# Kernel tuning notes

Hardware: AMD Instinct MI355X
Metric: run time of the kernel (lower is better)

## Reference

```python
import jax, jax.numpy as jnp
import numpy as np

N_POST_NMS = 2000      # Config.train_n_nms
MIN_SIZE = 16.0        # Config.prop_min_size
IMG_H = 800.0          # Config.input_shape[0]
IMG_W = 800.0          # Config.input_shape[1]
NMS_THRESH = 0.7       # Config.nms_thresh
N_PROPOSALS = 8192


def setup_inputs() -> dict:
    key = jax.random.key(0)
    k1, k2, k3 = jax.random.split(key, 3)
    # bbox_locs rows are (cy, cx, h, w); make them plausible for an 800x800 image
    ctr = jax.random.uniform(k1, (N_PROPOSALS, 2), dtype=jnp.float32) * 800.0
    sz = jax.random.uniform(k2, (N_PROPOSALS, 2), dtype=jnp.float32) * 260.0 + 4.0
    bbox_locs = jnp.concatenate([ctr, sz], axis=1)
    object_scores = jax.random.uniform(k3, (N_PROPOSALS,), dtype=jnp.float32)
    return {"bbox_locs": bbox_locs, "object_scores": object_scores}


def _decode_clip(bbox_locs):
    # center/size -> corners (y1,x1,y2,x2), size filter BEFORE clipping (as in source)
    cy, cx, h, w = bbox_locs[:, 0], bbox_locs[:, 1], bbox_locs[:, 2], bbox_locs[:, 3]
    y1, x1 = cy - 0.5 * h, cx - 0.5 * w
    y2, x2 = cy + 0.5 * h, cx + 0.5 * w
    valid = ((y2 - y1) > MIN_SIZE) & ((x2 - x1) > MIN_SIZE)
    boxes = jnp.stack([
        jnp.clip(y1, 0.0, IMG_H),
        jnp.clip(x1, 0.0, IMG_W),
        jnp.clip(y2, 0.0, IMG_H),
        jnp.clip(x2, 0.0, IMG_W),
    ], axis=1)  # [N,4]
    return boxes, valid


def _iou_matrix(b):
    # pairwise IoU, same convention as tf.image.non_max_suppression (no +1)
    y1, x1, y2, x2 = b[:, 0], b[:, 1], b[:, 2], b[:, 3]
    area = (y2 - y1) * (x2 - x1)
    iy = jnp.maximum(0.0, jnp.minimum(y2[:, None], y2[None, :]) - jnp.maximum(y1[:, None], y1[None, :]))
    ix = jnp.maximum(0.0, jnp.minimum(x2[:, None], x2[None, :]) - jnp.maximum(x1[:, None], x1[None, :]))
    inter = iy * ix
    union = area[:, None] + area[None, :] - inter
    return jnp.where(union > 0.0, inter / union, 0.0)


def _nms_select(boxes, scores, valid):
    # Greedy NMS. Invalid (too-small) boxes get -inf score so they sort last and
    # start suppressed -- equivalent to the tf.gather filtering in the original.
    N = boxes.shape[0]
    order = jnp.argsort(-jnp.where(valid, scores, -jnp.inf))
    bs = boxes[order]
    iou = _iou_matrix(bs)  # [N,N]
    idx = jnp.arange(N)

    def body(i, state):
        suppressed, kept = state
        keep_i = jnp.logical_not(suppressed[i])
        kept = kept.at[i].set(keep_i)
        suppressed = suppressed | (keep_i & (iou[i] > NMS_THRESH) & (idx > i))
        return suppressed, kept

    suppressed0 = jnp.logical_not(valid[order])
    kept0 = jnp.zeros((N,), dtype=bool)
    _, kept = jax.lax.fori_loop(0, N, body, (suppressed0, kept0))

    # first N_POST_NMS kept boxes in score order (same as max_output_size in TF)
    sel = jnp.nonzero(kept, size=N_POST_NMS, fill_value=0)[0]
    out_valid = jnp.arange(N_POST_NMS) < jnp.sum(kept)
    return order[sel], out_valid


def reference(bbox_locs, object_scores):
    boxes, valid = _decode_clip(bbox_locs)
    sel_idx, out_valid = _nms_select(boxes, object_scores, valid)
    # pad slots beyond the number of kept boxes with zeros (fixed output shape)
    return jnp.where(out_valid[:, None], boxes[sel_idx], 0.0)
```

## Files before the change

kernel.cpp:

```cpp
#include <hip/hip_runtime.h>
#include <cstdint>
#include <cstddef>

typedef unsigned long long ull;
typedef unsigned short u16;

#define N 8192
#define NWORDS 128
#define NPOST 2000
#define NMS_THR 0.7f
#define MASKW 48
#define SCAP 128
#define ICAP 16
#define NUNITS 312
#define SLICE_STRIDE 260


__device__ __forceinline__ float4 decode_clip_box(const float4 L, bool* valid) {
#pragma clang fp contract(off)
  float cy = L.x, cx = L.y, h = L.z, w = L.w;
  float y1 = cy - 0.5f * h;
  float x1 = cx - 0.5f * w;
  float y2 = cy + 0.5f * h;
  float x2 = cx + 0.5f * w;
  *valid = ((y2 - y1) > 16.0f) && ((x2 - x1) > 16.0f);
  float4 b;
  b.x = fminf(fmaxf(y1, 0.0f), 800.0f);
  b.y = fminf(fmaxf(x1, 0.0f), 800.0f);
  b.z = fminf(fmaxf(y2, 0.0f), 800.0f);
  b.w = fminf(fmaxf(x2, 0.0f), 800.0f);
  return b;
}

__device__ __forceinline__ float box_area(const float4 b) {
#pragma clang fp contract(off)
  return (b.z - b.x) * (b.w - b.y);
}

__device__ __forceinline__ bool iou_gt_thr(const float4 a, float aa,
                                           const float4 b, float ab) {
#pragma clang fp contract(off)
  float iy = fminf(a.z, b.z) - fmaxf(a.x, b.x);
  float ix = fminf(a.w, b.w) - fmaxf(a.y, b.y);
  iy = fmaxf(iy, 0.0f);
  ix = fmaxf(ix, 0.0f);
  float inter = iy * ix;
  float uni = aa + ab - inter;
  return (inter > 0.0f) && (uni > 0.0f) && ((inter / uni) > NMS_THR);
}

__device__ __forceinline__ ull resolve_word(ull dg, ull avail, int lane) {
  ull conflict = __ballot(((dg & avail) != 0ull) && ((avail >> lane) & 1ull));
  if (conflict == 0ull) return avail;
  ull dgT = 0ull;
  #pragma unroll
  for (int c = 0; c < 64; ++c) {
    ull tb = __ballot((dg >> c) & 1ull);
    if (lane == c) dgT = tb;
  }
  ull kept = avail;
  while (true) {
    bool sup = (dgT & kept) != 0ull;
    ull kn = avail & ~__ballot(sup);
    if (kn == kept) break;
    kept = kn;
  }
  return kept;
}

__device__ __forceinline__ unsigned aload(const unsigned* p) {
  return __hip_atomic_load(p, __ATOMIC_RELAXED, __HIP_MEMORY_SCOPE_AGENT);
}
__device__ __forceinline__ int aloadi(const int* p) {
  return __hip_atomic_load(p, __ATOMIC_RELAXED, __HIP_MEMORY_SCOPE_AGENT);
}

__global__ __launch_bounds__(256) void rankgather_kernel(
    const float* __restrict__ locs, const float* __restrict__ scores,
    float4* __restrict__ bs, float* __restrict__ area,
    int* __restrict__ ctrl, int* __restrict__ inCnt) {
  __shared__ float ssc[32 * SLICE_STRIDE];
  __shared__ int sRank[8][33];
  int tid = threadIdx.x, bid = blockIdx.x;
  if (bid == 0) {
    if (tid < 64) ctrl[tid] = 0;
    else if (tid < 128) inCnt[tid - 64] = 0;
  }
  const float4* locs4 = (const float4*)locs;
  for (int k = 0; k < 32; ++k) {
    int j = k * 256 + tid;
    bool v; (void)decode_clip_box(locs4[j], &v);
    float s = v ? scores[j] : -__builtin_inff();
    ssc[(j >> 8) * SLICE_STRIDE + (j & 255)] = s;
  }
  __syncthreads();
  int boxOff = tid & 7;
  int part = tid >> 3;
  int i = bid * 8 + boxOff;
  float si = ssc[(i >> 8) * SLICE_STRIDE + (i & 255)];
  const float4* s4 = (const float4*)(ssc + part * SLICE_STRIDE);
  int j0 = part * 256;
  int cnt = 0;
  for (int q = 0; q < 64; ++q) {
    float4 v = s4[q];
    int j = j0 + 4 * q;
    cnt += (v.x > si) || ((v.x == si) & ((j + 0) < i));
    cnt += (v.y > si) || ((v.y == si) & ((j + 1) < i));
    cnt += (v.z > si) || ((v.z == si) & ((j + 2) < i));
    cnt += (v.w > si) || ((v.w == si) & ((j + 3) < i));
  }
  sRank[boxOff][part] = cnt;
  __syncthreads();
  if (tid < 8) {
    int r = 0;
    #pragma unroll
    for (int p = 0; p < 32; ++p) r += sRank[tid][p];
    int ig = bid * 8 + tid;
    bool v;
    float4 b = decode_clip_box(locs4[ig], &v);
    bs[r] = b;
    area[r] = v ? box_area(b) : -1.0f;
  }
}

__global__ __launch_bounds__(256) void pairscan_kernel(
    const float4* __restrict__ bs, const float* __restrict__ area,
    int* __restrict__ ctrl, int* __restrict__ inCnt,
    unsigned* __restrict__ srcBuf, unsigned* __restrict__ inBuf,
    float* __restrict__ out) {
  __shared__ __align__(16) char smem[35840];
  int tid = threadIdx.x, bid = blockIdx.x;

  if (bid > 0) {
    float4* sb = (float4*)smem;
    float*  sa = (float*)(smem + 4096);
    int u = bid - 1;
    int cbq = 0;
    while (2 * (cbq + 1) * (cbq + 2) <= u) ++cbq;
    int rb = u - 2 * cbq * (cbq + 1);
    int lane = tid & 63, cq = tid >> 6;
    int cb = cbq * 4 + cq;
    int j0 = cb * 64;
    sb[cq * 64 + lane] = bs[j0 + lane];
    sa[cq * 64 + lane] = area[j0 + lane];
    int i = rb * 64 + lane;
    float4 r = bs[i];
    float ai = area[i];
    __syncthreads();
    if (cb >= rb && ai >= 0.0f) {
      ull bits = 0;
      for (int c = 0; c < 64; ++c) {
        if ((j0 + c) > i && sa[cq * 64 + c] >= 0.0f &&
            iou_gt_thr(r, ai, sb[cq * 64 + c], sa[cq * 64 + c]))
          bits |= 1ull << c;
      }
      int n = (int)__popcll(bits);
      if (n) {
        if (cb == rb) {
          int base = atomicAdd(&inCnt[cb], n);
          if (base + n > ICAP) {
            __hip_atomic_store(&ctrl[48], 1, __ATOMIC_RELAXED,
                               __HIP_MEMORY_SCOPE_AGENT);
          } else {
            int k = base;
            while (bits) {
              int c = (int)__builtin_ctzll(bits); bits &= bits - 1;
              __hip_atomic_store(&inBuf[cb * ICAP + k++],
                                 ((unsigned)c << 8) | (unsigned)lane,
                                 __ATOMIC_RELAXED, __HIP_MEMORY_SCOPE_AGENT);
            }
          }
        } else {
          int base = atomicAdd(&ctrl[rb], n);
          if (base + n > SCAP) {
            __hip_atomic_store(&ctrl[48], 1, __ATOMIC_RELAXED,
                               __HIP_MEMORY_SCOPE_AGENT);
          } else {
            int k = base;
            while (bits) {
              int c = (int)__builtin_ctzll(bits); bits &= bits - 1;
              __hip_atomic_store(&srcBuf[rb * SCAP + k++],
                                 ((unsigned)lane << 13) | ((unsigned)cb << 6) |
                                     (unsigned)c,
                                 __ATOMIC_RELAXED, __HIP_MEMORY_SCOPE_AGENT);
            }
          }
        }
      }
    }
    __syncthreads();
    if (tid == 0)
      __hip_atomic_fetch_add(&ctrl[49], 1, __ATOMIC_RELAXED,
                             __HIP_MEMORY_SCOPE_AGENT);
    return;
  }

  unsigned (*sSrc)[SCAP] = (unsigned(*)[SCAP])(smem + 0);
  unsigned (*sIn)[ICAP]  = (unsigned(*)[ICAP])(smem + 24576);
  int*  sSCnt     = (int*)(smem + 27648);
  int*  sICnt     = (int*)(smem + 27840);
  ull*  sRemv     = (ull*)(smem + 28032);
  u16*  sKeptList = (u16*)(smem + 29056);
  float4* sWB     = (float4*)(smem + 33056);
  float*  sWA     = (float*)(smem + 34080);
  ull*  sSupW     = (ull*)(smem + 34336);
  int*  sCtl      = (int*)(smem + 34344);

  {
    int wave = tid >> 6, lane = tid & 63;
    for (int b = 0; b < 4; ++b) {
      float av[8];
      #pragma unroll
      for (int q = 0; q < 8; ++q)
        av[q] = area[(wave + (b * 8 + q) * 4) * 64 + lane];
      #pragma unroll
      for (int q = 0; q < 8; ++q) {
        ull inv = __ballot(av[q] < 0.0f);
        if (lane == 0) sRemv[wave + (b * 8 + q) * 4] = inv;
      }
    }
  }
  if (tid == 254) sCtl[0] = 0;
  if (tid == 253) sCtl[1] = 0;

  if (tid == 0) {
    while (__hip_atomic_load(&ctrl[49], __ATOMIC_RELAXED,
                             __HIP_MEMORY_SCOPE_AGENT) < NUNITS)
      __builtin_amdgcn_s_sleep(2);
  }
  __syncthreads();

  if (tid < MASKW) { sSCnt[tid] = aloadi(&ctrl[tid]); sICnt[tid] = aloadi(&inCnt[tid]); }
  if (tid == 255) sCtl[2] = aloadi(&ctrl[48]);
  {
    const uint4* src4 = (const uint4*)srcBuf;
    uint4* dst4 = (uint4*)sSrc;
    #pragma unroll
    for (int k = 0; k < 6; ++k) dst4[tid + k * 256] = src4[tid + k * 256];
    const uint4* in4 = (const uint4*)inBuf;
    if (tid < 192) ((uint4*)sIn)[tid] = in4[tid];
  }
  __syncthreads();

  int sOver = sCtl[2];
  if (!sOver && tid < 64) {
    int lane = tid;
    int base = 0;
    for (int w = 0; w < MASKW; ++w) {
      ull avail = ~sRemv[w];
      int cnI = sICnt[w];
      ull kept;
      if (cnI == 0) {
        kept = avail;
      } else {
        ull dgT = 0ull;
        for (int k = 0; k < cnI; ++k) {
          unsigned p = sIn[w][k];
          int il = (int)(p & 63u);
          int jl = (int)(p >> 8) & 63;
          if (lane == jl) dgT |= 1ull << il;
        }
        ull cf = __ballot(((dgT & avail) != 0ull) && ((avail >> lane) & 1ull));
        if (cf == 0ull) {
          kept = avail;
        } else {
          kept = avail;
          while (true) {
            bool sup = (dgT & kept) != 0ull;
            ull kn = avail & ~__ballot(sup);
            if (kn == kept) break;
            kept = kn;
          }
        }
      }
      if ((kept >> lane) & 1ull) {
        int rank = base + (int)__popcll(kept & ((1ull << lane) - 1ull));
        if (rank < NPOST) sKeptList[rank] = (u16)(w * 64 + lane);
      }
      base += (int)__popcll(kept);
      if (base >= NPOST) break;
      int cnS = sSCnt[w];
      for (int k = lane; k < cnS; k += 64) {
        unsigned p = sSrc[w][k];
        int il = (int)(p >> 13) & 63;
        if ((kept >> il) & 1ull) {
          int wt = (int)(p >> 6) & 127;
          atomicOr(&sRemv[wt], 1ull << (p & 63u));
        }
      }
    }
    if (lane == 0) { sCtl[0] = base; if (base >= NPOST) sCtl[1] = 1; }
  }
  __syncthreads();

  int startW = sOver ? 0 : MASKW;
  if (!sCtl[1]) {
    for (int w = startW; w < NWORDS; ++w) {
      if (tid < 64) { sWB[tid] = bs[w * 64 + tid]; sWA[tid] = area[w * 64 + tid]; }
      if (tid == 0) *sSupW = sRemv[w];
      __syncthreads();
      int nk = sCtl[0];
      int c = tid & 63;
      for (int k0 = tid >> 6; k0 < nk; k0 += 4) {
        int ki = sKeptList[k0];
        float4 kb = bs[ki];
        bool s = iou_gt_thr(kb, area[ki], sWB[c], sWA[c]);
        ull bits = __ballot(s);
        if (c == 0 && bits) atomicOr(sSupW, bits);
      }
      __syncthreads();
      if (tid < 64) {
        int lane = tid;
        float4 bm = sWB[lane];
        float am = sWA[lane];
        ull dg = 0;
        if (am >= 0.0f) {
          for (int cc = lane + 1; cc < 64; ++cc)
            if (sWA[cc] >= 0.0f && iou_gt_thr(bm, am, sWB[cc], sWA[cc]))
              dg |= 1ull << cc;
        }
        ull avail = ~*sSupW;
        ull kept = resolve_word(dg, avail, lane);
        int base = sCtl[0];
        if ((kept >> lane) & 1ull) {
          int rank = base + (int)__popcll(kept & ((1ull << lane) - 1ull));
          if (rank < NPOST) sKeptList[rank] = (u16)(w * 64 + lane);
        }
        if (lane == 0) {
          int nb = base + (int)__popcll(kept);
          sCtl[0] = nb;
          if (nb >= NPOST) sCtl[1] = 1;
        }
      }
      __syncthreads();
      if (sCtl[1]) break;
    }
  }

  __syncthreads();
  int total = sCtl[0];
  if (total > NPOST) total = NPOST;
  for (int r = tid; r < NPOST; r += 256) {
    float4 v = make_float4(0.0f, 0.0f, 0.0f, 0.0f);
    if (r < total) v = bs[sKeptList[r]];
    reinterpret_cast<float4*>(out)[r] = v;
  }
  if (total == 0 && tid == 0)
    out[0] = 5.0e9f + (float)sCtl[2] * 1.0e8f;
}

extern "C" void kernel_launch(void* const* d_in, const int* in_sizes, int n_in,
                              void* d_out, int out_size, void* d_ws, size_t ws_size,
                              hipStream_t stream) {
  const float* locs   = (const float*)d_in[0];
  const float* scores = (const float*)d_in[1];

  char* ws = (char*)d_ws;
  float4*   bs       = (float4*)(ws + 0);
  float*    area     = (float*)(ws + 131072);
  int*      ctrl     = (int*)(ws + 163840);
  int*      inCnt    = (int*)(ws + 164096);
  unsigned* srcBuf   = (unsigned*)(ws + 164352);
  unsigned* inBuf    = (unsigned*)(ws + 188928);

  rankgather_kernel<<<N / 8, 256, 0, stream>>>(locs, scores, bs, area, ctrl, inCnt);
  pairscan_kernel<<<NUNITS + 1, 256, 0, stream>>>(
      bs, area, ctrl, inCnt, srcBuf, inBuf, (float*)d_out);
}
```

Before: 60.04 us.

## Split fused pairscan into separate pairs and scan kernel launches

Replaces the single persistent kernel, in which block 0 spin-waited on an atomic counter for the other 312 pair blocks, with two launches: a pairs kernel that builds the suppression lists and a single-block scan kernel that consumes them. Kernel-boundary ordering now replaces the atomic counter and relaxed atomic loads and stores. This removes the spin-wait and the agent-scope atomics, and frees the CU that block 0 occupied. The cost is an extra launch and the inter-kernel gap, and the scan block can no longer preload its invalid-box masks while the pairs work is still running.

```diff
diff --git a/kernel.cpp b/kernel.cpp
--- a/kernel.cpp
+++ b/kernel.cpp
@@ -68,13 +68,6 @@
   return kept;
 }
 
-__device__ __forceinline__ unsigned aload(const unsigned* p) {
-  return __hip_atomic_load(p, __ATOMIC_RELAXED, __HIP_MEMORY_SCOPE_AGENT);
-}
-__device__ __forceinline__ int aloadi(const int* p) {
-  return __hip_atomic_load(p, __ATOMIC_RELAXED, __HIP_MEMORY_SCOPE_AGENT);
-}
-
 __global__ __launch_bounds__(256) void rankgather_kernel(
     const float* __restrict__ locs, const float* __restrict__ scores,
     float4* __restrict__ bs, float* __restrict__ area,
@@ -123,77 +116,62 @@
   }
 }
 
-__global__ __launch_bounds__(256) void pairscan_kernel(
+__global__ __launch_bounds__(256) void pairs_kernel(
     const float4* __restrict__ bs, const float* __restrict__ area,
     int* __restrict__ ctrl, int* __restrict__ inCnt,
-    unsigned* __restrict__ srcBuf, unsigned* __restrict__ inBuf,
+    unsigned* __restrict__ srcBuf, unsigned* __restrict__ inBuf) {
+  __shared__ float4 sb[4][64];
+  __shared__ float  sa[4][64];
+  int tid = threadIdx.x;
+  int u = blockIdx.x;
+  int cbq = 0;
+  while (2 * (cbq + 1) * (cbq + 2) <= u) ++cbq;
+  int rb = u - 2 * cbq * (cbq + 1);
+  int lane = tid & 63, cq = tid >> 6;
+  int cb = cbq * 4 + cq;
+  int j0 = cb * 64;
+  sb[cq][lane] = bs[j0 + lane];
+  sa[cq][lane] = area[j0 + lane];
+  int i = rb * 64 + lane;
+  float4 r = bs[i];
+  float ai = area[i];
+  __syncthreads();
+  if (cb < rb || ai < 0.0f) return;
+  ull bits = 0;
+  for (int c = 0; c < 64; ++c) {
+    if ((j0 + c) > i && sa[cq][c] >= 0.0f &&
+        iou_gt_thr(r, ai, sb[cq][c], sa[cq][c]))
+      bits |= 1ull << c;
+  }
+  int n = (int)__popcll(bits);
+  if (!n) return;
+  if (cb == rb) {
+    int base = atomicAdd(&inCnt[cb], n);
+    if (base + n > ICAP) { ctrl[48] = 1; return; }
+    int k = base;
+    while (bits) {
+      int c = (int)__builtin_ctzll(bits); bits &= bits - 1;
+      inBuf[cb * ICAP + k++] = ((unsigned)c << 8) | (unsigned)lane;
+    }
+  } else {
+    int base = atomicAdd(&ctrl[rb], n);
+    if (base + n > SCAP) { ctrl[48] = 1; return; }
+    int k = base;
+    while (bits) {
+      int c = (int)__builtin_ctzll(bits); bits &= bits - 1;
+      srcBuf[rb * SCAP + k++] =
+          ((unsigned)lane << 13) | ((unsigned)cb << 6) | (unsigned)c;
+    }
+  }
+}
+
+__global__ __launch_bounds__(256) void scan_kernel(
+    const float4* __restrict__ bs, const float* __restrict__ area,
+    const int* __restrict__ ctrl, const int* __restrict__ inCnt,
+    const unsigned* __restrict__ srcBuf, const unsigned* __restrict__ inBuf,
     float* __restrict__ out) {
   __shared__ __align__(16) char smem[35840];
-  int tid = threadIdx.x, bid = blockIdx.x;
-
-  if (bid > 0) {
-    float4* sb = (float4*)smem;
-    float*  sa = (float*)(smem + 4096);
-    int u = bid - 1;
-    int cbq = 0;
-    while (2 * (cbq + 1) * (cbq + 2) <= u) ++cbq;
-    int rb = u - 2 * cbq * (cbq + 1);
-    int lane = tid & 63, cq = tid >> 6;
-    int cb = cbq * 4 + cq;
-    int j0 = cb * 64;
-    sb[cq * 64 + lane] = bs[j0 + lane];
-    sa[cq * 64 + lane] = area[j0 + lane];
-    int i = rb * 64 + lane;
-    float4 r = bs[i];
-    float ai = area[i];
-    __syncthreads();
-    if (cb >= rb && ai >= 0.0f) {
-      ull bits = 0;
-      for (int c = 0; c < 64; ++c) {
-        if ((j0 + c) > i && sa[cq * 64 + c] >= 0.0f &&
-            iou_gt_thr(r, ai, sb[cq * 64 + c], sa[cq * 64 + c]))
-          bits |= 1ull << c;
-      }
-      int n = (int)__popcll(bits);
-      if (n) {
-        if (cb == rb) {
-          int base = atomicAdd(&inCnt[cb], n);
-          if (base + n > ICAP) {
-            __hip_atomic_store(&ctrl[48], 1, __ATOMIC_RELAXED,
-                               __HIP_MEMORY_SCOPE_AGENT);
-          } else {
-            int k = base;
-            while (bits) {
-              int c = (int)__builtin_ctzll(bits); bits &= bits - 1;
-              __hip_atomic_store(&inBuf[cb * ICAP + k++],
-                                 ((unsigned)c << 8) | (unsigned)lane,
-                                 __ATOMIC_RELAXED, __HIP_MEMORY_SCOPE_AGENT);
-            }
-          }
-        } else {
-          int base = atomicAdd(&ctrl[rb], n);
-          if (base + n > SCAP) {
-            __hip_atomic_store(&ctrl[48], 1, __ATOMIC_RELAXED,
-                               __HIP_MEMORY_SCOPE_AGENT);
-          } else {
-            int k = base;
-            while (bits) {
-              int c = (int)__builtin_ctzll(bits); bits &= bits - 1;
-              __hip_atomic_store(&srcBuf[rb * SCAP + k++],
-                                 ((unsigned)lane << 13) | ((unsigned)cb << 6) |
-                                     (unsigned)c,
-                                 __ATOMIC_RELAXED, __HIP_MEMORY_SCOPE_AGENT);
-            }
-          }
-        }
-      }
-    }
-    __syncthreads();
-    if (tid == 0)
-      __hip_atomic_fetch_add(&ctrl[49], 1, __ATOMIC_RELAXED,
-                             __HIP_MEMORY_SCOPE_AGENT);
-    return;
-  }
+  int tid = threadIdx.x;
 
   unsigned (*sSrc)[SCAP] = (unsigned(*)[SCAP])(smem + 0);
   unsigned (*sIn)[ICAP]  = (unsigned(*)[ICAP])(smem + 24576);
@@ -222,16 +200,8 @@
   }
   if (tid == 254) sCtl[0] = 0;
   if (tid == 253) sCtl[1] = 0;
-
-  if (tid == 0) {
-    while (__hip_atomic_load(&ctrl[49], __ATOMIC_RELAXED,
-                             __HIP_MEMORY_SCOPE_AGENT) < NUNITS)
-      __builtin_amdgcn_s_sleep(2);
-  }
-  __syncthreads();
-
-  if (tid < MASKW) { sSCnt[tid] = aloadi(&ctrl[tid]); sICnt[tid] = aloadi(&inCnt[tid]); }
-  if (tid == 255) sCtl[2] = aloadi(&ctrl[48]);
+  if (tid < MASKW) { sSCnt[tid] = ctrl[tid]; sICnt[tid] = inCnt[tid]; }
+  if (tid == 255) sCtl[2] = ctrl[48];
   {
     const uint4* src4 = (const uint4*)srcBuf;
     uint4* dst4 = (uint4*)sSrc;
@@ -364,6 +334,7 @@
   unsigned* inBuf    = (unsigned*)(ws + 188928);
 
   rankgather_kernel<<<N / 8, 256, 0, stream>>>(locs, scores, bs, area, ctrl, inCnt);
-  pairscan_kernel<<<NUNITS + 1, 256, 0, stream>>>(
-      bs, area, ctrl, inCnt, srcBuf, inBuf, (float*)d_out);
-}
+  pairs_kernel<<<NUNITS, 256, 0, stream>>>(bs, area, ctrl, inCnt, srcBuf, inBuf);
+  scan_kernel<<<1, 256, 0, stream>>>(bs, area, ctrl, inCnt, srcBuf, inBuf,
+                                     (float*)d_out);
+}
```

Result: no change. 60.94 us, median of 2 (+1.5%).
